# Optimization experiments

Hardware: AMD Instinct MI355X
Metric: run time of the kernel (lower is better)

## Reference

```python
import jax, jax.numpy as jnp
import numpy as np

NEG = -1e9  # stand-in for 'entry does not exist' (saliency <= 0)


def upsample_bilinear_align_corners(x, scale=8):
    # x: [N, C, H, W] -> [N, C, H*scale, W*scale], matches F.interpolate(..., mode='bilinear', align_corners=True)
    N, C, H, W = x.shape
    Ho, Wo = H * scale, W * scale
    ys = jnp.linspace(0.0, H - 1.0, Ho)
    xs = jnp.linspace(0.0, W - 1.0, Wo)
    y0 = jnp.floor(ys).astype(jnp.int32)
    y1 = jnp.minimum(y0 + 1, H - 1)
    wy = (ys - y0).reshape(1, 1, Ho, 1)
    x0 = jnp.floor(xs).astype(jnp.int32)
    x1 = jnp.minimum(x0 + 1, W - 1)
    wx = (xs - x0).reshape(1, 1, 1, Wo)
    r = x[:, :, y0, :] * (1.0 - wy) + x[:, :, y1, :] * wy      # interp along H
    return r[:, :, :, x0] * (1.0 - wx) + r[:, :, :, x1] * wx   # interp along W


def setup_inputs() -> dict:
    key = jax.random.key(0)
    k0, k1, k2, k3 = jax.random.split(key, 4)
    N, C, H, W = 1, 64, 80, 80
    return {
        "feat_reg_vi": jax.random.normal(k0, (N, C, H, W), jnp.float32),
        "feat_reg_ir": jax.random.normal(k1, (N, C, H, W), jnp.float32),
        "feat_sa_vi": jax.random.normal(k2, (N, 1, H, W), jnp.float32),
        "feat_sa_ir": jax.random.normal(k3, (N, 1, H, W), jnp.float32),
    }


def reference(feat_reg_vi, feat_reg_ir, feat_sa_vi, feat_sa_ir):
    N, C, H, W = feat_reg_vi.shape
    L = H * W
    # saliency validity masks (original: torch.where(sa > 0) index selection)
    valid_vi = feat_sa_vi.reshape(N, L) > 0.0
    valid_ir = feat_sa_ir.reshape(N, L) > 0.0
    # n_c_h_w_2_n_hw_c + / sqrt(C)
    fv = feat_reg_vi.reshape(N, C, L).transpose(0, 2, 1) / (C ** 0.5)  # [N, L, C]
    fi = feat_reg_ir.reshape(N, C, L).transpose(0, 2, 1) / (C ** 0.5)  # [N, S, C]
    conf = jnp.einsum('nlc,nsc->nls', fv, fi) / 0.1                    # [N, L, S]
    # mask out rows/cols that the original would have dropped
    conf = jnp.where(valid_vi[:, :, None] & valid_ir[:, None, :], conf, NEG)
    # mutual nearest-neighbor masking
    row_max = conf.max(axis=2, keepdims=True)
    col_max = conf.max(axis=1, keepdims=True)
    mutual = ((conf == row_max) & (conf == col_max)).astype(conf.dtype)
    mask = jnp.where(conf > 0.0, mutual, jnp.zeros_like(conf))
    mask_v = mask.max(axis=2)                # [N, L]  (1.0 where row i has a match)
    all_j = jnp.argmax(mask, axis=2)         # [N, L]  matched column per row
    # dense (static-shape) analogue of the variable-length index extraction
    idx = jnp.arange(L)
    mkpts0 = jnp.stack([idx % W, idx // W], axis=1) * 8            # [L, 2]
    mkpts1 = jnp.stack([all_j % W, all_j // W], axis=2) * 8        # [N, L, 2]
    score = jnp.take_along_axis(conf, all_j[:, :, None], axis=2)[:, :, 0] * mask_v  # [N, L]
    sa_ir_up = upsample_bilinear_align_corners(feat_sa_ir, 8)      # [N, 1, 8H, 8W]
    return (mkpts0, mkpts1, mask_v, score, sa_ir_up)
```

## Files before the change

### kernel.cpp

```cpp
#include <hip/hip_runtime.h>

#define LDIM 6400
#define CDIM 64
#define WDIM 80
#define NEGV -1e9f
#define SCALE 0.15625f

typedef unsigned short u16;
typedef unsigned long long u64;
typedef __attribute__((ext_vector_type(8))) short bf16x8;
typedef __attribute__((ext_vector_type(4))) float f32x4;
typedef __attribute__((ext_vector_type(4))) unsigned uint4e;

#define ROWP_OFF 0
#define COLE_OFF (LDIM * 8)
#define AHI_OFF  (COLE_OFF + LDIM * 4)
#define ARR_BYTES (LDIM * CDIM * 2)
#define ALO_OFF  (AHI_OFF + ARR_BYTES)
#define BHI_OFF  (ALO_OFF + ARR_BYTES)
#define BLO_OFF  (BHI_OFF + ARR_BYTES)
#define WS_NEEDED (BLO_OFF + ARR_BYTES)

__device__ __forceinline__ unsigned encf(float f) {
    unsigned b = __float_as_uint(f);
    return (b & 0x80000000u) ? ~b : (b | 0x80000000u);
}
__device__ __forceinline__ float decf(unsigned e) {
    unsigned b = (e & 0x80000000u) ? (e ^ 0x80000000u) : ~e;
    return __uint_as_float(b);
}

__device__ __forceinline__ void splitbf(float a, u16& h, u16& l) {
    unsigned ub = __float_as_uint(a);
    unsigned hb = ub & 0xFFFF0000u;
    float lof = a - __uint_as_float(hb);
    unsigned lb_ = __float_as_uint(lof);
    h = (u16)(hb >> 16);
    l = (u16)((lb_ + 0x7FFFu + ((lb_ >> 16) & 1u)) >> 16);
}

typedef __attribute__((address_space(1))) const unsigned as1_u32;
typedef __attribute__((address_space(3))) unsigned as3_u32;
__device__ __forceinline__ void gl_lds16(const u16* g, u16* l) {
    __builtin_amdgcn_global_load_lds((as1_u32*)g, (as3_u32*)l, 16, 0, 0);
}

__global__ __launch_bounds__(256) void prep_kernel(
        const float* __restrict__ A, const float* __restrict__ B,
        u16* __restrict__ Ahi, u16* __restrict__ Alo,
        u16* __restrict__ Bhi, u16* __restrict__ Blo,
        u64* __restrict__ rowp, unsigned* __restrict__ colenc,
        float* __restrict__ out) {
    int idx = blockIdx.x;
    const float* src;
    u16 *dhi, *dlo;
    bool isA = idx < 200;
    int u = isA ? idx : idx - 200;
    if (isA) { src = A; dhi = Ahi; dlo = Alo; }
    else     { src = B; dhi = Bhi; dlo = Blo; }
    const int bi = u >> 1;
    const int khalf = u & 1;
    const int t = threadIdx.x;
    const int l = bi * 64 + (t & 63);
    const int grp = t >> 6;
    const int kq = khalf * 2 + (grp & 1);
    const int mh = grp >> 1;
    const int ks = kq >> 1;
    const int g = (kq & 1) * 2 + mh;

    unsigned hp[4], lp[4];
    #pragma unroll
    for (int mm = 0; mm < 4; ++mm) {
        int k = kq * 16 + 2 * (mh * 4 + mm);
        u16 h0, l0, h1, l1;
        splitbf(src[k * LDIM + l], h0, l0);
        splitbf(src[(k + 1) * LDIM + l], h1, l1);
        hp[mm] = (unsigned)h0 | ((unsigned)h1 << 16);
        lp[mm] = (unsigned)l0 | ((unsigned)l1 << 16);
    }
    size_t base = (size_t)(l >> 4) * 1024 + (size_t)ks * 512 + (size_t)(l & 15) * 8
                  + (size_t)g * 128;
    *(uint4e*)(dhi + base) = (uint4e){hp[0], hp[1], hp[2], hp[3]};
    *(uint4e*)(dlo + base) = (uint4e){lp[0], lp[1], lp[2], lp[3]};

    if (isA && khalf == 0 && grp == 0) {
        rowp[l] = 0ull;
        colenc[l] = 0u;
        out[2 * l]     = (float)((l % WDIM) * 8);
        out[2 * l + 1] = (float)((l / WDIM) * 8);
    }
}

__global__ __launch_bounds__(512, 4) void main_mfma(
        const u16* __restrict__ Ahi, const u16* __restrict__ Alo,
        const u16* __restrict__ Bhi, const u16* __restrict__ Blo,
        const float* __restrict__ sav, const float* __restrict__ sai,
        u64* __restrict__ rowp, unsigned* __restrict__ colenc,
        float* __restrict__ out) {
    const int tid = threadIdx.x;
    const int b = blockIdx.x;

    if (b >= 2500) {
        int i = (b - 2500) * 512 + tid;
        int oy = i / 640, ox = i % 640;
        const float step = 79.0f / 639.0f;
        float fy = (float)oy * step;
        float fx = (float)ox * step;
        int y0 = (int)floorf(fy); if (y0 > 79) y0 = 79; if (y0 < 0) y0 = 0;
        int x0 = (int)floorf(fx); if (x0 > 79) x0 = 79; if (x0 < 0) x0 = 0;
        int y1 = (y0 + 1 < 80) ? y0 + 1 : 79;
        int x1 = (x0 + 1 < 80) ? x0 + 1 : 79;
        float wy = fy - (float)y0;
        float wx = fx - (float)x0;
        float v00 = sai[y0 * 80 + x0], v01 = sai[y0 * 80 + x1];
        float v10 = sai[y1 * 80 + x0], v11 = sai[y1 * 80 + x1];
        float r0 = v00 * (1.0f - wy) + v10 * wy;
        float r1 = v01 * (1.0f - wy) + v11 * wy;
        out[38400 + i] = r0 * (1.0f - wx) + r1 * wx;
        return;
    }

    __attribute__((aligned(16))) __shared__ char smem[34816];
    u16* sAh = (u16*)smem;
    u16* sAl = (u16*)(smem + 16384);
    u64  (*rowbuf)[17] = (u64 (*)[17])smem;
    float (*colbuf)[33] = (float (*)[33])(smem + 17408);

    const int lb = (b / 50) * 128;
    const int sb = (b % 50) * 128;
    const int lane = tid & 63, wid = tid >> 6;
    const int l15 = lane & 15, g = lane >> 4;
    const int lhalf = wid >> 2, sq = wid & 3;

    {
        const u16* Ah_pan = Ahi + (size_t)(lb >> 4) * 1024;
        const u16* Al_pan = Alo + (size_t)(lb >> 4) * 1024;
        #pragma unroll
        for (int c = 0; c < 2; ++c) {
            int chunk = wid * 2 + c;
            gl_lds16(Ah_pan + chunk * 512 + lane * 8, sAh + chunk * 512);
            gl_lds16(Al_pan + chunk * 512 + lane * 8, sAl + chunk * 512);
        }
    }

    const u16* pBh = Bhi + (size_t)(sb / 16 + sq * 2) * 1024 + lane * 8;
    const u16* pBl = Blo + (size_t)(sb / 16 + sq * 2) * 1024 + lane * 8;

    bf16x8 bh0[2], bl0[2];
    #pragma unroll
    for (int j = 0; j < 2; ++j) {
        bh0[j] = *(const bf16x8*)(pBh + (size_t)j * 1024);
        bl0[j] = *(const bf16x8*)(pBl + (size_t)j * 1024);
    }
    bool rok[4];
    #pragma unroll
    for (int i = 0; i < 4; ++i)
        rok[i] = sav[lb + lhalf * 64 + i * 16 + l15] > 0.0f;
    bool cok[2][4];
    #pragma unroll
    for (int j = 0; j < 2; ++j)
        #pragma unroll
        for (int r = 0; r < 4; ++r)
            cok[j][r] = sai[sb + sq * 32 + j * 16 + g * 4 + r] > 0.0f;

    f32x4 acc[4][2];
    #pragma unroll
    for (int i = 0; i < 4; ++i)
        #pragma unroll
        for (int j = 0; j < 2; ++j)
            #pragma unroll
            for (int e = 0; e < 4; ++e) acc[i][j][e] = 0.0f;

    const int aoff = (lhalf * 4) * 1024 + lane * 8;

    __syncthreads();

    bf16x8 bh1[2], bl1[2];
    #pragma unroll
    for (int j = 0; j < 2; ++j) {
        bh1[j] = *(const bf16x8*)(pBh + (size_t)j * 1024 + 512);
        bl1[j] = *(const bf16x8*)(pBl + (size_t)j * 1024 + 512);
    }

    {
        bf16x8 ah[4], al[4];
        #pragma unroll
        for (int i = 0; i < 4; ++i) {
            ah[i] = *(const bf16x8*)(sAh + aoff + i * 1024);
            al[i] = *(const bf16x8*)(sAl + aoff + i * 1024);
        }
        #pragma unroll
        for (int i = 0; i < 4; ++i)
            #pragma unroll
            for (int j = 0; j < 2; ++j) {
                acc[i][j] = __builtin_amdgcn_mfma_f32_16x16x32_bf16(bh0[j], ah[i], acc[i][j], 0, 0, 0);
                acc[i][j] = __builtin_amdgcn_mfma_f32_16x16x32_bf16(bh0[j], al[i], acc[i][j], 0, 0, 0);
                acc[i][j] = __builtin_amdgcn_mfma_f32_16x16x32_bf16(bl0[j], ah[i], acc[i][j], 0, 0, 0);
            }
    }
    {
        bf16x8 ah[4], al[4];
        #pragma unroll
        for (int i = 0; i < 4; ++i) {
            ah[i] = *(const bf16x8*)(sAh + aoff + i * 1024 + 512);
            al[i] = *(const bf16x8*)(sAl + aoff + i * 1024 + 512);
        }
        #pragma unroll
        for (int i = 0; i < 4; ++i)
            #pragma unroll
            for (int j = 0; j < 2; ++j) {
                acc[i][j] = __builtin_amdgcn_mfma_f32_16x16x32_bf16(bh1[j], ah[i], acc[i][j], 0, 0, 0);
                acc[i][j] = __builtin_amdgcn_mfma_f32_16x16x32_bf16(bh1[j], al[i], acc[i][j], 0, 0, 0);
                acc[i][j] = __builtin_amdgcn_mfma_f32_16x16x32_bf16(bl1[j], ah[i], acc[i][j], 0, 0, 0);
            }
    }

    #pragma unroll
    for (int i = 0; i < 4; ++i)
        #pragma unroll
        for (int j = 0; j < 2; ++j)
            #pragma unroll
            for (int r = 0; r < 4; ++r)
                acc[i][j][r] = (rok[i] && cok[j][r]) ? acc[i][j][r] * SCALE : NEGV;

    __syncthreads();

    #pragma unroll
    for (int i = 0; i < 4; ++i) {
        float v = acc[i][0][0];
        int ci = sb + sq * 32 + g * 4;
        #pragma unroll
        for (int j = 0; j < 2; ++j)
            #pragma unroll
            for (int r = 0; r < 4; ++r) {
                if (j == 0 && r == 0) continue;
                float x = acc[i][j][r];
                int cx = sb + sq * 32 + j * 16 + g * 4 + r;
                bool up = x > v;
                v = up ? x : v;
                ci = up ? cx : ci;
            }
        rowbuf[lhalf * 64 + i * 16 + l15][sq * 4 + g] =
            ((u64)encf(v) << 32) | (unsigned)(~(unsigned)ci);
    }

    #pragma unroll
    for (int j = 0; j < 2; ++j)
        #pragma unroll
        for (int r = 0; r < 4; ++r) {
            float m = acc[0][j][r];
            #pragma unroll
            for (int i = 1; i < 4; ++i) m = fmaxf(m, acc[i][j][r]);
            colbuf[sq * 32 + j * 16 + g * 4 + r][lhalf * 16 + l15] = m;
        }

    __syncthreads();

    if (tid < 128) {
        u64 m = rowbuf[tid][0];
        #pragma unroll
        for (int e = 1; e < 16; ++e) {
            u64 x = rowbuf[tid][e];
            m = (x > m) ? x : m;
        }
        atomicMax(&rowp[lb + tid], m);
    } else if (tid < 256) {
        int c = tid - 128;
        float m = colbuf[c][0];
        #pragma unroll
        for (int e = 1; e < 32; ++e) m = fmaxf(m, colbuf[c][e]);
        atomicMax(&colenc[sb + c], encf(m));
    }
}

__global__ void finalize_kernel(const u64* __restrict__ rowp,
                                const unsigned* __restrict__ colenc,
                                float* __restrict__ out) {
    int l = blockIdx.x * 256 + threadIdx.x;
    if (l >= LDIM) return;
    u64 p = rowp[l];
    unsigned enc = (unsigned)(p >> 32);
    unsigned s = ~((unsigned)p);
    float val = decf(enc);
    bool mk = (enc == colenc[s]) && (val > 0.0f);
    int aj = mk ? (int)s : 0;
    out[12800 + 2 * l]     = (float)((aj % WDIM) * 8);
    out[12800 + 2 * l + 1] = (float)((aj / WDIM) * 8);
    out[25600 + l] = mk ? 1.0f : 0.0f;
    out[32000 + l] = mk ? val : 0.0f;
}


__global__ void init_kernel(u64* __restrict__ rowp,
                            unsigned* __restrict__ colenc,
                            float* __restrict__ out) {
    int i = blockIdx.x * 256 + threadIdx.x;
    if (i < LDIM) {
        rowp[i] = 0ull;
        colenc[i] = 0u;
        out[2 * i]     = (float)((i % WDIM) * 8);
        out[2 * i + 1] = (float)((i / WDIM) * 8);
    }
}

__global__ __launch_bounds__(256, 4) void main_kernel(
        const float* __restrict__ A, const float* __restrict__ B,
        const float* __restrict__ sav, const float* __restrict__ sai,
        u64* __restrict__ rowp, unsigned* __restrict__ colenc,
        float* __restrict__ out) {
    __shared__ float As[32][128];
    __shared__ float Bs[32][128];
    const int tid = threadIdx.x;
    const int b = blockIdx.x;

    if (b >= 2500) {
        int i = (b - 2500) * 256 + tid;
        int oy = i / 640, ox = i % 640;
        const float step = 79.0f / 639.0f;
        float fy = (float)oy * step;
        float fx = (float)ox * step;
        int y0 = (int)floorf(fy); if (y0 > 79) y0 = 79; if (y0 < 0) y0 = 0;
        int x0 = (int)floorf(fx); if (x0 > 79) x0 = 79; if (x0 < 0) x0 = 0;
        int y1 = (y0 + 1 < 80) ? y0 + 1 : 79;
        int x1 = (x0 + 1 < 80) ? x0 + 1 : 79;
        float wy = fy - (float)y0;
        float wx = fx - (float)x0;
        float v00 = sai[y0 * 80 + x0], v01 = sai[y0 * 80 + x1];
        float v10 = sai[y1 * 80 + x0], v11 = sai[y1 * 80 + x1];
        float r0 = v00 * (1.0f - wy) + v10 * wy;
        float r1 = v01 * (1.0f - wy) + v11 * wy;
        out[38400 + i] = r0 * (1.0f - wx) + r1 * wx;
        return;
    }

    const int lb = (b / 50) * 128;
    const int sb = (b % 50) * 128;
    const int tx = tid & 15, ty = tid >> 4;

    float acc[8][8];
    #pragma unroll
    for (int i = 0; i < 8; ++i)
        #pragma unroll
        for (int j = 0; j < 8; ++j) acc[i][j] = 0.0f;

    float4* As4 = (float4*)As;
    float4* Bs4 = (float4*)Bs;
    const float4* pA = (const float4*)As;
    const float4* pB = (const float4*)Bs;

    for (int kb = 0; kb < 2; ++kb) {
        #pragma unroll
        for (int i = tid, it = 0; it < 4; i += 256, ++it) {
            int c = i >> 5, q = i & 31;
            As4[i] = ((const float4*)(A + (kb * 32 + c) * LDIM + lb))[q];
            Bs4[i] = ((const float4*)(B + (kb * 32 + c) * LDIM + sb))[q];
        }
        __syncthreads();

        #pragma unroll 4
        for (int c = 0; c < 32; ++c) {
            float4 a0 = pA[(c << 5) + ty];
            float4 a1 = pA[(c << 5) + ty + 16];
            float4 b0 = pB[(c << 5) + tx];
            float4 b1 = pB[(c << 5) + tx + 16];
            float av[8] = {a0.x, a0.y, a0.z, a0.w, a1.x, a1.y, a1.z, a1.w};
            float bv[8] = {b0.x, b0.y, b0.z, b0.w, b1.x, b1.y, b1.z, b1.w};
            #pragma unroll
            for (int i = 0; i < 8; ++i)
                #pragma unroll
                for (int j = 0; j < 8; ++j)
                    acc[i][j] = fmaf(av[i], bv[j], acc[i][j]);
        }
        __syncthreads();
    }

    int rg[8], cg[8];
    #pragma unroll
    for (int i = 0; i < 8; ++i) {
        rg[i] = lb + ty * 4 + ((i < 4) ? i : (64 + i - 4));
        cg[i] = sb + tx * 4 + ((i < 4) ? i : (64 + i - 4));
    }
    bool rok[8], cok[8];
    #pragma unroll
    for (int i = 0; i < 8; ++i) rok[i] = sav[rg[i]] > 0.0f;
    #pragma unroll
    for (int j = 0; j < 8; ++j) cok[j] = sai[cg[j]] > 0.0f;

    float conf[8][8];
    #pragma unroll
    for (int i = 0; i < 8; ++i)
        #pragma unroll
        for (int j = 0; j < 8; ++j)
            conf[i][j] = (rok[i] && cok[j]) ? acc[i][j] * 0.15625f : NEGV;

    #pragma unroll
    for (int i = 0; i < 8; ++i) {
        float v = conf[i][0];
        int ci = cg[0];
        #pragma unroll
        for (int j = 1; j < 8; ++j) {
            bool up = conf[i][j] > v;
            v = up ? conf[i][j] : v;
            ci = up ? cg[j] : ci;
        }
        #pragma unroll
        for (int d = 1; d < 16; d <<= 1) {
            float ov = __shfl_xor(v, d, 64);
            int oi = __shfl_xor(ci, d, 64);
            bool take = (ov > v) || ((ov == v) && (oi < ci));
            v = take ? ov : v;
            ci = take ? oi : ci;
        }
        if (tx == 0)
            atomicMax(&rowp[rg[i]],
                      ((u64)encf(v) << 32) | (unsigned)(~(unsigned)ci));
    }

    __syncthreads();
    float* cred = &As[0][0];
    #pragma unroll
    for (int j = 0; j < 8; ++j) {
        float m = conf[0][j];
        #pragma unroll
        for (int i = 1; i < 8; ++i) m = fmaxf(m, conf[i][j]);
        int cl = tx * 4 + ((j < 4) ? j : (64 + j - 4));
        cred[cl * 17 + ty] = m;
    }
    __syncthreads();
    if (tid < 128) {
        float m = cred[tid * 17];
        #pragma unroll
        for (int t = 1; t < 16; ++t) m = fmaxf(m, cred[tid * 17 + t]);
        atomicMax(&colenc[sb + tid], encf(m));
    }
}

extern "C" void kernel_launch(void* const* d_in, const int* in_sizes, int n_in,
                              void* d_out, int out_size, void* d_ws, size_t ws_size,
                              hipStream_t stream) {
    const float* frv = (const float*)d_in[0];
    const float* fri = (const float*)d_in[1];
    const float* sav = (const float*)d_in[2];
    const float* sai = (const float*)d_in[3];
    float* out = (float*)d_out;
    char* ws = (char*)d_ws;

    u64* rowp = (u64*)(ws + ROWP_OFF);
    unsigned* colenc = (unsigned*)(ws + COLE_OFF);

    if (ws_size >= (size_t)WS_NEEDED) {
        u16* Ahi = (u16*)(ws + AHI_OFF);
        u16* Alo = (u16*)(ws + ALO_OFF);
        u16* Bhi = (u16*)(ws + BHI_OFF);
        u16* Blo = (u16*)(ws + BLO_OFF);
        prep_kernel<<<400, 256, 0, stream>>>(frv, fri, Ahi, Alo, Bhi, Blo,
                                             rowp, colenc, out);
        main_mfma<<<3300, 512, 0, stream>>>(Ahi, Alo, Bhi, Blo, sav, sai,
                                            rowp, colenc, out);
        finalize_kernel<<<25, 256, 0, stream>>>(rowp, colenc, out);
    } else {
        init_kernel<<<25, 256, 0, stream>>>(rowp, colenc, out);
        main_kernel<<<4100, 256, 0, stream>>>(frv, fri, sav, sai,
                                              rowp, colenc, out);
        finalize_kernel<<<25, 256, 0, stream>>>(rowp, colenc, out);
    }
}
```

Measured before the change: 89.43 us.

## Stage B tiles through LDS and move upsample work into prep kernel

The B operand panels (hi/lo bf16 splits) are now loaded into shared memory with async global-to-LDS copies, alongside A, instead of each wave reading them from global memory into registers. The bilinear upsample blocks move from the main MFMA kernel into the prep kernel, so the main grid contains only matmul tiles. LDS use per block grows from about 34 KB to 64 KB, which may reduce how many blocks fit per CU, and the prep kernel grows to 2000 blocks.

```diff
diff --git a/kernel.cpp b/kernel.cpp
--- a/kernel.cpp
+++ b/kernel.cpp
@@ -49,9 +49,34 @@
         const float* __restrict__ A, const float* __restrict__ B,
         u16* __restrict__ Ahi, u16* __restrict__ Alo,
         u16* __restrict__ Bhi, u16* __restrict__ Blo,
+        const float* __restrict__ sai,
         u64* __restrict__ rowp, unsigned* __restrict__ colenc,
         float* __restrict__ out) {
     int idx = blockIdx.x;
+    const int t = threadIdx.x;
+
+    if (idx >= 400) {
+        int i = (idx - 400) * 256 + t;
+        if (i < 409600) {
+            int oy = i / 640, ox = i % 640;
+            const float step = 79.0f / 639.0f;
+            float fy = (float)oy * step;
+            float fx = (float)ox * step;
+            int y0 = (int)floorf(fy); if (y0 > 79) y0 = 79; if (y0 < 0) y0 = 0;
+            int x0 = (int)floorf(fx); if (x0 > 79) x0 = 79; if (x0 < 0) x0 = 0;
+            int y1 = (y0 + 1 < 80) ? y0 + 1 : 79;
+            int x1 = (x0 + 1 < 80) ? x0 + 1 : 79;
+            float wy = fy - (float)y0;
+            float wx = fx - (float)x0;
+            float v00 = sai[y0 * 80 + x0], v01 = sai[y0 * 80 + x1];
+            float v10 = sai[y1 * 80 + x0], v11 = sai[y1 * 80 + x1];
+            float r0 = v00 * (1.0f - wy) + v10 * wy;
+            float r1 = v01 * (1.0f - wy) + v11 * wy;
+            out[38400 + i] = r0 * (1.0f - wx) + r1 * wx;
+        }
+        return;
+    }
+
     const float* src;
     u16 *dhi, *dlo;
     bool isA = idx < 200;
@@ -60,7 +85,6 @@
     else     { src = B; dhi = Bhi; dlo = Blo; }
     const int bi = u >> 1;
     const int khalf = u & 1;
-    const int t = threadIdx.x;
     const int l = bi * 64 + (t & 63);
     const int grp = t >> 6;
     const int kq = khalf * 2 + (grp & 1);
@@ -100,29 +124,11 @@
     const int tid = threadIdx.x;
     const int b = blockIdx.x;
 
-    if (b >= 2500) {
-        int i = (b - 2500) * 512 + tid;
-        int oy = i / 640, ox = i % 640;
-        const float step = 79.0f / 639.0f;
-        float fy = (float)oy * step;
-        float fx = (float)ox * step;
-        int y0 = (int)floorf(fy); if (y0 > 79) y0 = 79; if (y0 < 0) y0 = 0;
-        int x0 = (int)floorf(fx); if (x0 > 79) x0 = 79; if (x0 < 0) x0 = 0;
-        int y1 = (y0 + 1 < 80) ? y0 + 1 : 79;
-        int x1 = (x0 + 1 < 80) ? x0 + 1 : 79;
-        float wy = fy - (float)y0;
-        float wx = fx - (float)x0;
-        float v00 = sai[y0 * 80 + x0], v01 = sai[y0 * 80 + x1];
-        float v10 = sai[y1 * 80 + x0], v11 = sai[y1 * 80 + x1];
-        float r0 = v00 * (1.0f - wy) + v10 * wy;
-        float r1 = v01 * (1.0f - wy) + v11 * wy;
-        out[38400 + i] = r0 * (1.0f - wx) + r1 * wx;
-        return;
-    }
-
-    __attribute__((aligned(16))) __shared__ char smem[34816];
+    __attribute__((aligned(16))) __shared__ char smem[65536];
     u16* sAh = (u16*)smem;
     u16* sAl = (u16*)(smem + 16384);
+    u16* sBh = (u16*)(smem + 32768);
+    u16* sBl = (u16*)(smem + 49152);
     u64  (*rowbuf)[17] = (u64 (*)[17])smem;
     float (*colbuf)[33] = (float (*)[33])(smem + 17408);
 
@@ -135,23 +141,18 @@
     {
         const u16* Ah_pan = Ahi + (size_t)(lb >> 4) * 1024;
         const u16* Al_pan = Alo + (size_t)(lb >> 4) * 1024;
+        const u16* Bh_pan = Bhi + (size_t)(sb >> 4) * 1024;
+        const u16* Bl_pan = Blo + (size_t)(sb >> 4) * 1024;
         #pragma unroll
         for (int c = 0; c < 2; ++c) {
             int chunk = wid * 2 + c;
             gl_lds16(Ah_pan + chunk * 512 + lane * 8, sAh + chunk * 512);
             gl_lds16(Al_pan + chunk * 512 + lane * 8, sAl + chunk * 512);
-        }
-    }
-
-    const u16* pBh = Bhi + (size_t)(sb / 16 + sq * 2) * 1024 + lane * 8;
-    const u16* pBl = Blo + (size_t)(sb / 16 + sq * 2) * 1024 + lane * 8;
-
-    bf16x8 bh0[2], bl0[2];
-    #pragma unroll
-    for (int j = 0; j < 2; ++j) {
-        bh0[j] = *(const bf16x8*)(pBh + (size_t)j * 1024);
-        bl0[j] = *(const bf16x8*)(pBl + (size_t)j * 1024);
-    }
+            gl_lds16(Bh_pan + chunk * 512 + lane * 8, sBh + chunk * 512);
+            gl_lds16(Bl_pan + chunk * 512 + lane * 8, sBl + chunk * 512);
+        }
+    }
+
     bool rok[4];
     #pragma unroll
     for (int i = 0; i < 4; ++i)
@@ -172,46 +173,30 @@
             for (int e = 0; e < 4; ++e) acc[i][j][e] = 0.0f;
 
     const int aoff = (lhalf * 4) * 1024 + lane * 8;
+    const int boff = (sq * 2) * 1024 + lane * 8;
 
     __syncthreads();
 
-    bf16x8 bh1[2], bl1[2];
-    #pragma unroll
-    for (int j = 0; j < 2; ++j) {
-        bh1[j] = *(const bf16x8*)(pBh + (size_t)j * 1024 + 512);
-        bl1[j] = *(const bf16x8*)(pBl + (size_t)j * 1024 + 512);
-    }
-
-    {
-        bf16x8 ah[4], al[4];
+    #pragma unroll
+    for (int ks = 0; ks < 2; ++ks) {
+        bf16x8 ah[4], al[4], bh[2], bl[2];
+        #pragma unroll
+        for (int j = 0; j < 2; ++j) {
+            bh[j] = *(const bf16x8*)(sBh + boff + j * 1024 + ks * 512);
+            bl[j] = *(const bf16x8*)(sBl + boff + j * 1024 + ks * 512);
+        }
         #pragma unroll
         for (int i = 0; i < 4; ++i) {
-            ah[i] = *(const bf16x8*)(sAh + aoff + i * 1024);
-            al[i] = *(const bf16x8*)(sAl + aoff + i * 1024);
+            ah[i] = *(const bf16x8*)(sAh + aoff + i * 1024 + ks * 512);
+            al[i] = *(const bf16x8*)(sAl + aoff + i * 1024 + ks * 512);
         }
         #pragma unroll
         for (int i = 0; i < 4; ++i)
             #pragma unroll
             for (int j = 0; j < 2; ++j) {
-                acc[i][j] = __builtin_amdgcn_mfma_f32_16x16x32_bf16(bh0[j], ah[i], acc[i][j], 0, 0, 0);
-                acc[i][j] = __builtin_amdgcn_mfma_f32_16x16x32_bf16(bh0[j], al[i], acc[i][j], 0, 0, 0);
-                acc[i][j] = __builtin_amdgcn_mfma_f32_16x16x32_bf16(bl0[j], ah[i], acc[i][j], 0, 0, 0);
-            }
-    }
-    {
-        bf16x8 ah[4], al[4];
-        #pragma unroll
-        for (int i = 0; i < 4; ++i) {
-            ah[i] = *(const bf16x8*)(sAh + aoff + i * 1024 + 512);
-            al[i] = *(const bf16x8*)(sAl + aoff + i * 1024 + 512);
-        }
-        #pragma unroll
-        for (int i = 0; i < 4; ++i)
-            #pragma unroll
-            for (int j = 0; j < 2; ++j) {
-                acc[i][j] = __builtin_amdgcn_mfma_f32_16x16x32_bf16(bh1[j], ah[i], acc[i][j], 0, 0, 0);
-                acc[i][j] = __builtin_amdgcn_mfma_f32_16x16x32_bf16(bh1[j], al[i], acc[i][j], 0, 0, 0);
-                acc[i][j] = __builtin_amdgcn_mfma_f32_16x16x32_bf16(bl1[j], ah[i], acc[i][j], 0, 0, 0);
+                acc[i][j] = __builtin_amdgcn_mfma_f32_16x16x32_bf16(bh[j], ah[i], acc[i][j], 0, 0, 0);
+                acc[i][j] = __builtin_amdgcn_mfma_f32_16x16x32_bf16(bh[j], al[i], acc[i][j], 0, 0, 0);
+                acc[i][j] = __builtin_amdgcn_mfma_f32_16x16x32_bf16(bl[j], ah[i], acc[i][j], 0, 0, 0);
             }
     }
 
@@ -453,9 +438,9 @@
         u16* Alo = (u16*)(ws + ALO_OFF);
         u16* Bhi = (u16*)(ws + BHI_OFF);
         u16* Blo = (u16*)(ws + BLO_OFF);
-        prep_kernel<<<400, 256, 0, stream>>>(frv, fri, Ahi, Alo, Bhi, Blo,
-                                             rowp, colenc, out);
-        main_mfma<<<3300, 512, 0, stream>>>(Ahi, Alo, Bhi, Blo, sav, sai,
+        prep_kernel<<<2000, 256, 0, stream>>>(frv, fri, Ahi, Alo, Bhi, Blo,
+                                              sai, rowp, colenc, out);
+        main_mfma<<<2500, 512, 0, stream>>>(Ahi, Alo, Bhi, Blo, sav, sai,
                                             rowp, colenc, out);
         finalize_kernel<<<25, 256, 0, stream>>>(rowp, colenc, out);
     } else {
```

Result: no change. 88.89 us (-0.6%).
